# Optimization experiments

Hardware: AMD Instinct MI355X
Metric: run time of the kernel (lower is better)

## Reference

```python
import jax, jax.numpy as jnp
import numpy as np

CONF_THRESH = 0.5
EPS = 1e-7  # tf.keras.backend.epsilon()

B, H, W = 32, 512, 512


def setup_inputs() -> dict:
    key = jax.random.key(0)
    ks = jax.random.split(key, 6)
    region_true = jax.random.uniform(ks[0], (B, H, W), dtype=jnp.float32)
    affinity_true = jax.random.uniform(ks[1], (B, H, W), dtype=jnp.float32)
    region_pred = jax.random.uniform(ks[2], (B, H, W), dtype=jnp.float32)
    affinity_pred = jax.random.uniform(ks[3], (B, H, W), dtype=jnp.float32)
    confidence = jax.random.uniform(ks[4], (B, H, W), dtype=jnp.float32)
    fg = (jax.random.uniform(ks[5], (B, H, W)) < 0.1).astype(jnp.float32)
    bg = 1.0 - fg
    return {
        "region_true": region_true,
        "affinity_true": affinity_true,
        "region_pred": region_pred,
        "affinity_pred": affinity_pred,
        "confidence": confidence,
        "fg_mask": fg,
        "bg_mask": bg,
    }


def reference(region_true, affinity_true, region_pred, affinity_pred,
              confidence, fg_mask, bg_mask):
    # confidence gating
    conf = jnp.where(confidence >= CONF_THRESH, confidence, jnp.zeros_like(confidence))
    # masked L1 losses (region + affinity)
    l_total = (jnp.abs(region_true - region_pred)
               + jnp.abs(affinity_true - affinity_pred)) * conf  # [B,H,W]
    # OHEM: original code clamps neg_num = min(bg_num, 3*fg_num, 1), so
    # top_k with k<=1 -> threshold is the per-sample MAX of bg-masked loss.
    neg_loss = l_total * bg_mask
    thresh = jnp.max(neg_loss.reshape(neg_loss.shape[0], -1), axis=-1)  # [B]
    hard_bg_mask = ((bg_mask > 0)
                    & (neg_loss >= thresh[:, None, None])).astype(jnp.float32)
    train_mask = hard_bg_mask + fg_mask
    return jnp.sum(l_total * train_mask) / (jnp.sum(conf * train_mask) + EPS)
```

## Files before the change

### kernel.cpp

```cpp
#include <hip/hip_runtime.h>


#define HW_TOTAL (512 * 512)
#define NBATCH 32
#define BLOCKS_PER_IMG 64
#define CHUNK 4096
#define THREADS 256

__device__ __forceinline__ float f4_get(const float4& v, int j) {
    return j == 0 ? v.x : (j == 1 ? v.y : (j == 2 ? v.z : v.w));
}

__global__ __launch_bounds__(THREADS) void craft_pass1(
    const float* __restrict__ RT, const float* __restrict__ AT,
    const float* __restrict__ RP, const float* __restrict__ AP,
    const float* __restrict__ CF, const float* __restrict__ FG,
    float* __restrict__ recs)
{
    const int b = blockIdx.x >> 6;
    const int chunk = blockIdx.x & 63;
    const size_t base = (size_t)b * HW_TOTAL + (size_t)chunk * CHUNK;

    const float4* rt4 = (const float4*)(RT + base);
    const float4* at4 = (const float4*)(AT + base);
    const float4* rp4 = (const float4*)(RP + base);
    const float4* ap4 = (const float4*)(AP + base);
    const float4* cf4 = (const float4*)(CF + base);
    const float4* fg4 = (const float4*)(FG + base);

    float m = 0.0f, sl = 0.0f, sc = 0.0f, fl = 0.0f, fc = 0.0f;

    #pragma unroll
    for (int it = 0; it < 4; ++it) {
        const int i = it * THREADS + threadIdx.x;
        const float4 rt = rt4[i], at = at4[i], rp = rp4[i], ap = ap4[i];
        const float4 cf = cf4[i], fg = fg4[i];
        #pragma unroll
        for (int j = 0; j < 4; ++j) {
            const float cfv = f4_get(cf, j);
            const float c = (cfv >= 0.5f) ? cfv : 0.0f;
            const float l = (fabsf(f4_get(rt, j) - f4_get(rp, j)) +
                             fabsf(f4_get(at, j) - f4_get(ap, j))) * c;
            const float fgv = f4_get(fg, j);
            fl += l * fgv;
            fc += c * fgv;
            if (fgv == 0.0f) {
                const float v = l;
                if (v > m)       { m = v; sl = l; sc = c; }
                else if (v == m) { sl += l; sc += c; }
            }
        }
    }

    #pragma unroll
    for (int off = 1; off < 64; off <<= 1) {
        const float om  = __shfl_xor(m,  off, 64);
        const float osl = __shfl_xor(sl, off, 64);
        const float osc = __shfl_xor(sc, off, 64);
        fl += __shfl_xor(fl, off, 64);
        fc += __shfl_xor(fc, off, 64);
        if (om > m)       { m = om; sl = osl; sc = osc; }
        else if (om == m) { sl += osl; sc += osc; }
    }

    __shared__ float sm[4], ssl[4], ssc[4], sfl[4], sfc[4];
    const int lane = threadIdx.x & 63;
    const int wave = threadIdx.x >> 6;
    if (lane == 0) { sm[wave] = m; ssl[wave] = sl; ssc[wave] = sc;
                     sfl[wave] = fl; sfc[wave] = fc; }
    __syncthreads();
    if (threadIdx.x == 0) {
        #pragma unroll
        for (int w = 1; w < 4; ++w) {
            if (sm[w] > m)       { m = sm[w]; sl = ssl[w]; sc = ssc[w]; }
            else if (sm[w] == m) { sl += ssl[w]; sc += ssc[w]; }
            fl += sfl[w];
            fc += sfc[w];
        }
        float* r = recs + (size_t)blockIdx.x * 5;
        r[0] = m; r[1] = sl; r[2] = sc; r[3] = fl; r[4] = fc;
    }
}

__global__ __launch_bounds__(1024) void craft_pass2(
    const float* __restrict__ recs, float* __restrict__ out)
{
    __shared__ float snum[NBATCH], sden[NBATCH];
    const int lane = threadIdx.x & 63;
    const int wave = threadIdx.x >> 6;

    for (int b = wave; b < NBATCH; b += 16) {
        const float* r = recs + ((size_t)(b * BLOCKS_PER_IMG + lane)) * 5;
        float m = r[0], sl = r[1], sc = r[2], fl = r[3], fc = r[4];
        #pragma unroll
        for (int off = 1; off < 64; off <<= 1) {
            const float om  = __shfl_xor(m,  off, 64);
            const float osl = __shfl_xor(sl, off, 64);
            const float osc = __shfl_xor(sc, off, 64);
            fl += __shfl_xor(fl, off, 64);
            fc += __shfl_xor(fc, off, 64);
            if (om > m)       { m = om; sl = osl; sc = osc; }
            else if (om == m) { sl += osl; sc += osc; }
        }
        if (lane == 0) { snum[b] = sl + fl; sden[b] = sc + fc; }
    }
    __syncthreads();
    if (threadIdx.x == 0) {
        float num = 0.0f, den = 0.0f;
        #pragma unroll
        for (int i = 0; i < NBATCH; ++i) { num += snum[i]; den += sden[i]; }
        out[0] = num / (den + 1e-7f);
    }
}

extern "C" void kernel_launch(void* const* d_in, const int* in_sizes, int n_in,
                              void* d_out, int out_size, void* d_ws, size_t ws_size,
                              hipStream_t stream) {
    const float* RT = (const float*)d_in[0];
    const float* AT = (const float*)d_in[1];
    const float* RP = (const float*)d_in[2];
    const float* AP = (const float*)d_in[3];
    const float* CF = (const float*)d_in[4];
    const float* FG = (const float*)d_in[5];
    float* out = (float*)d_out;
    float* recs = (float*)d_ws;

    craft_pass1<<<NBATCH * BLOCKS_PER_IMG, THREADS, 0, stream>>>(
        RT, AT, RP, AP, CF, FG, recs);
    craft_pass2<<<1, 1024, 0, stream>>>(recs, out);
}
```

Measured before the change: 40.31 us.

## Fuse final reduction into main kernel via last-block atomic counter

Merges the two-kernel reduction into a single kernel. Each block publishes its partial record and increments a global atomic counter, and the last block to arrive performs the cross-block reduction and writes the output. Records are stored structure-of-arrays so the final loads are coalesced. The goal is to remove the second kernel launch and its dependency gap, at the cost of a memset launch to reset the counter and a serialized tail reduction done by a single 256-thread block.

```diff
diff --git a/kernel.cpp b/kernel.cpp
--- a/kernel.cpp
+++ b/kernel.cpp
@@ -4,18 +4,21 @@
 #define HW_TOTAL (512 * 512)
 #define NBATCH 32
 #define BLOCKS_PER_IMG 64
+#define NBLOCKS (NBATCH * BLOCKS_PER_IMG)
 #define CHUNK 4096
 #define THREADS 256
+#define RSTRIDE NBLOCKS
 
 __device__ __forceinline__ float f4_get(const float4& v, int j) {
     return j == 0 ? v.x : (j == 1 ? v.y : (j == 2 ? v.z : v.w));
 }
 
-__global__ __launch_bounds__(THREADS) void craft_pass1(
+__global__ __launch_bounds__(THREADS) void craft_fused(
     const float* __restrict__ RT, const float* __restrict__ AT,
     const float* __restrict__ RP, const float* __restrict__ AP,
     const float* __restrict__ CF, const float* __restrict__ FG,
-    float* __restrict__ recs)
+    float* __restrict__ recs, unsigned int* __restrict__ counter,
+    float* __restrict__ out)
 {
     const int b = blockIdx.x >> 6;
     const int chunk = blockIdx.x & 63;
@@ -64,6 +67,7 @@
     }
 
     __shared__ float sm[4], ssl[4], ssc[4], sfl[4], sfc[4];
+    __shared__ unsigned int s_old;
     const int lane = threadIdx.x & 63;
     const int wave = threadIdx.x >> 6;
     if (lane == 0) { sm[wave] = m; ssl[wave] = sl; ssc[wave] = sc;
@@ -77,32 +81,43 @@
             fl += sfl[w];
             fc += sfc[w];
         }
-        float* r = recs + (size_t)blockIdx.x * 5;
-        r[0] = m; r[1] = sl; r[2] = sc; r[3] = fl; r[4] = fc;
+        recs[0 * RSTRIDE + blockIdx.x] = m;
+        recs[1 * RSTRIDE + blockIdx.x] = sl;
+        recs[2 * RSTRIDE + blockIdx.x] = sc;
+        recs[3 * RSTRIDE + blockIdx.x] = fl;
+        recs[4 * RSTRIDE + blockIdx.x] = fc;
+        __threadfence();
+        s_old = __hip_atomic_fetch_add(counter, 1u, __ATOMIC_ACQ_REL,
+                                       __HIP_MEMORY_SCOPE_AGENT);
     }
-}
+    __syncthreads();
+    if (s_old != NBLOCKS - 1) return;
 
-__global__ __launch_bounds__(1024) void craft_pass2(
-    const float* __restrict__ recs, float* __restrict__ out)
-{
+    __threadfence();
     __shared__ float snum[NBATCH], sden[NBATCH];
-    const int lane = threadIdx.x & 63;
-    const int wave = threadIdx.x >> 6;
-
-    for (int b = wave; b < NBATCH; b += 16) {
-        const float* r = recs + ((size_t)(b * BLOCKS_PER_IMG + lane)) * 5;
-        float m = r[0], sl = r[1], sc = r[2], fl = r[3], fc = r[4];
+    for (int bb = wave; bb < NBATCH; bb += 4) {
+        const int idx = bb * BLOCKS_PER_IMG + lane;
+        float m2  = __hip_atomic_load(&recs[0 * RSTRIDE + idx],
+                                      __ATOMIC_RELAXED, __HIP_MEMORY_SCOPE_AGENT);
+        float sl2 = __hip_atomic_load(&recs[1 * RSTRIDE + idx],
+                                      __ATOMIC_RELAXED, __HIP_MEMORY_SCOPE_AGENT);
+        float sc2 = __hip_atomic_load(&recs[2 * RSTRIDE + idx],
+                                      __ATOMIC_RELAXED, __HIP_MEMORY_SCOPE_AGENT);
+        float fl2 = __hip_atomic_load(&recs[3 * RSTRIDE + idx],
+                                      __ATOMIC_RELAXED, __HIP_MEMORY_SCOPE_AGENT);
+        float fc2 = __hip_atomic_load(&recs[4 * RSTRIDE + idx],
+                                      __ATOMIC_RELAXED, __HIP_MEMORY_SCOPE_AGENT);
         #pragma unroll
         for (int off = 1; off < 64; off <<= 1) {
-            const float om  = __shfl_xor(m,  off, 64);
-            const float osl = __shfl_xor(sl, off, 64);
-            const float osc = __shfl_xor(sc, off, 64);
-            fl += __shfl_xor(fl, off, 64);
-            fc += __shfl_xor(fc, off, 64);
-            if (om > m)       { m = om; sl = osl; sc = osc; }
-            else if (om == m) { sl += osl; sc += osc; }
+            const float om  = __shfl_xor(m2,  off, 64);
+            const float osl = __shfl_xor(sl2, off, 64);
+            const float osc = __shfl_xor(sc2, off, 64);
+            fl2 += __shfl_xor(fl2, off, 64);
+            fc2 += __shfl_xor(fc2, off, 64);
+            if (om > m2)       { m2 = om; sl2 = osl; sc2 = osc; }
+            else if (om == m2) { sl2 += osl; sc2 += osc; }
         }
-        if (lane == 0) { snum[b] = sl + fl; sden[b] = sc + fc; }
+        if (lane == 0) { snum[bb] = sl2 + fl2; sden[bb] = sc2 + fc2; }
     }
     __syncthreads();
     if (threadIdx.x == 0) {
@@ -124,8 +139,10 @@
     const float* FG = (const float*)d_in[5];
     float* out = (float*)d_out;
     float* recs = (float*)d_ws;
+    unsigned int* counter = (unsigned int*)((char*)d_ws + NBLOCKS * 5 * sizeof(float));
 
-    craft_pass1<<<NBATCH * BLOCKS_PER_IMG, THREADS, 0, stream>>>(
-        RT, AT, RP, AP, CF, FG, recs);
-    craft_pass2<<<1, 1024, 0, stream>>>(recs, out);
+    hipMemsetAsync(counter, 0, sizeof(unsigned int), stream);
+
+    craft_fused<<<NBLOCKS, THREADS, 0, stream>>>(
+        RT, AT, RP, AP, CF, FG, recs, counter, out);
 }
```

Measured after the change: 154.7 us. 3.84x slower.
